# Kernel tuning notes

Measured on AMD Instinct MI355X. Metric: run time of the kernel, lower is better.

Reference implementation:

```python
import jax, jax.numpy as jnp
import numpy as np

D_MODEL = 1024
NUM_HEADS = 16
HEAD_DIM = D_MODEL // NUM_HEADS


def setup_inputs() -> dict:
    key = jax.random.key(0)
    ks = jax.random.split(key, 11)
    B, S = 4, 2048
    s = 1.0 / np.sqrt(D_MODEL)
    inp = {
        'query': jax.random.normal(ks[0], (B, S, D_MODEL), jnp.float32),
        'key': jax.random.normal(ks[1], (B, S, D_MODEL), jnp.float32),
        'value': jax.random.normal(ks[2], (B, S, D_MODEL), jnp.float32),
        'W_q': jax.random.normal(ks[3], (D_MODEL, D_MODEL), jnp.float32) * s,
        'b_q': jnp.zeros((D_MODEL,), jnp.float32),
        'W_k': jax.random.normal(ks[4], (D_MODEL, D_MODEL), jnp.float32) * s,
        'b_k': jnp.zeros((D_MODEL,), jnp.float32),
        'W_v': jax.random.normal(ks[5], (D_MODEL, D_MODEL), jnp.float32) * s,
        'b_v': jnp.zeros((D_MODEL,), jnp.float32),
        'W_o': jax.random.normal(ks[6], (D_MODEL, D_MODEL), jnp.float32) * s,
        'b_o': jnp.zeros((D_MODEL,), jnp.float32),
    }
    return inp


def reference(query, key, value, W_q, b_q, W_k, b_k, W_v, b_v, W_o, b_o):
    B, S, _ = query.shape
    # Linear projections (torch Linear: x @ W.T + b)
    Q = query @ W_q.T + b_q
    K = key @ W_k.T + b_k
    V = value @ W_v.T + b_v
    # [B, H, S, Dh]
    def split_heads(x):
        return x.reshape(B, -1, NUM_HEADS, HEAD_DIM).transpose(0, 2, 1, 3)
    Qh, Kh, Vh = split_heads(Q), split_heads(K), split_heads(V)
    scale = 1.0 / jnp.sqrt(jnp.float32(HEAD_DIM))
    scores = jnp.einsum('bhqd,bhkd->bhqk', Qh, Kh) * scale
    attn = jax.nn.softmax(scores, axis=-1)
    out = jnp.einsum('bhqk,bhkd->bhqd', attn, Vh)
    out = out.transpose(0, 2, 1, 3).reshape(B, S, D_MODEL)
    return out @ W_o.T + b_o
```

## Files before the change

### kernel.cpp

```cpp
#include <hip/hip_runtime.h>


#define BATCH 4
#define SEQ   2048
#define NH    16
#define DH    64
#define DM    1024
#define LOG2E 1.4426950408889634f
#define CSC   (0.125f * LOG2E)

typedef __attribute__((ext_vector_type(8))) short s16x8;
typedef __attribute__((ext_vector_type(4))) float f32x4;
typedef const __attribute__((address_space(1))) unsigned int* gas1;
typedef __attribute__((address_space(3))) unsigned int* las3;

__device__ __forceinline__ unsigned short f2bf(float f) {
  unsigned int u = __float_as_uint(f);
  u += 0x7FFFu + ((u >> 16) & 1u);
  return (unsigned short)(u >> 16);
}

__device__ __forceinline__ unsigned int cvt_pk_bf16(float lo, float hi) {
  unsigned int r;
  asm("v_cvt_pk_bf16_f32 %0, %1, %2" : "=v"(r) : "v"(lo), "v"(hi));
  return r;
}

__global__ __launch_bounds__(256) void cvt3_k(const float* __restrict__ s0,
                                              const float* __restrict__ s1,
                                              const float* __restrict__ s2,
                                              unsigned short* __restrict__ d0,
                                              unsigned short* __restrict__ d1,
                                              unsigned short* __restrict__ d2, int n4) {
  const float* s = blockIdx.y == 0 ? s0 : blockIdx.y == 1 ? s1 : s2;
  unsigned short* d = blockIdx.y == 0 ? d0 : blockIdx.y == 1 ? d1 : d2;
  int i = blockIdx.x * 256 + threadIdx.x;
  if (i < n4) {
    float4 v = ((const float4*)s)[i];
    ushort4 o;
    o.x = f2bf(v.x); o.y = f2bf(v.y); o.z = f2bf(v.z); o.w = f2bf(v.w);
    ((ushort4*)d)[i] = o;
  }
}

__global__ __launch_bounds__(256) void cvt4_k(const float* __restrict__ s0,
                                              const float* __restrict__ s1,
                                              const float* __restrict__ s2,
                                              const float* __restrict__ s3,
                                              unsigned short* __restrict__ d0,
                                              unsigned short* __restrict__ d1,
                                              unsigned short* __restrict__ d2,
                                              unsigned short* __restrict__ d3, int n4) {
  const float* s = blockIdx.y == 0 ? s0 : blockIdx.y == 1 ? s1 : blockIdx.y == 2 ? s2 : s3;
  unsigned short* d = blockIdx.y == 0 ? d0 : blockIdx.y == 1 ? d1 : blockIdx.y == 2 ? d2 : d3;
  int i = blockIdx.x * 256 + threadIdx.x;
  if (i < n4) {
    float4 v = ((const float4*)s)[i];
    ushort4 o;
    o.x = f2bf(v.x); o.y = f2bf(v.y); o.z = f2bf(v.z); o.w = f2bf(v.w);
    ((ushort4*)d)[i] = o;
  }
}

template<bool BIAS_ROW, bool OUT_F32>
__device__ __forceinline__ void gemm_core(const unsigned short* __restrict__ A,
                                          const unsigned short* __restrict__ Bm,
                                          const float* __restrict__ bias,
                                          void* __restrict__ Cout,
                                          int M, int N, int K, int tM, int tN,
                                          unsigned short* As, unsigned short* Bs) {
  const int tid = threadIdx.x;
  const int wave = tid >> 6, lane = tid & 63;
  const int lr = lane & 15, lh = lane >> 4;
  const int wm = (wave >> 1) * 64, wn = (wave & 1) * 64;
  f32x4 acc[4][4] = {};

  for (int k0 = 0; k0 < K; k0 += 64) {
    __syncthreads();
#pragma unroll
    for (int i = 0; i < 4; ++i) {
      const int slot = wave * 256 + i * 64 + lane;
      const int row = slot >> 3;
      const int cg = (slot & 7) ^ (row & 7);
      const unsigned short* ga = A  + (size_t)(tM * 128 + row) * K + k0 + cg * 8;
      const unsigned short* gb = Bm + (size_t)(tN * 128 + row) * K + k0 + cg * 8;
      __builtin_amdgcn_global_load_lds((gas1)ga, (las3)(As + (wave * 256 + i * 64) * 8), 16, 0, 0);
      __builtin_amdgcn_global_load_lds((gas1)gb, (las3)(Bs + (wave * 256 + i * 64) * 8), 16, 0, 0);
    }
    __syncthreads();

    s16x8 af[4][2], bfr[4][2];
#pragma unroll
    for (int mt = 0; mt < 4; ++mt) {
#pragma unroll
      for (int kt = 0; kt < 2; ++kt) {
        const int ra = wm + mt * 16 + lr;
        af[mt][kt] = *(const s16x8*)(As + ra * 64 + (((kt * 4 + lh) ^ (ra & 7)) * 8));
        const int rb = wn + mt * 16 + lr;
        bfr[mt][kt] = *(const s16x8*)(Bs + rb * 64 + (((kt * 4 + lh) ^ (rb & 7)) * 8));
      }
    }
#pragma unroll
    for (int mt = 0; mt < 4; ++mt) {
#pragma unroll
      for (int nt = 0; nt < 4; ++nt) {
        acc[mt][nt] = __builtin_amdgcn_mfma_f32_16x16x32_bf16(af[mt][0], bfr[nt][0], acc[mt][nt], 0, 0, 0);
        acc[mt][nt] = __builtin_amdgcn_mfma_f32_16x16x32_bf16(af[mt][1], bfr[nt][1], acc[mt][nt], 0, 0, 0);
      }
    }
  }

#pragma unroll
  for (int mt = 0; mt < 4; ++mt) {
#pragma unroll
    for (int nt = 0; nt < 4; ++nt) {
      const int row0 = tM * 128 + wm + mt * 16 + lh * 4;
      const int col  = tN * 128 + wn + nt * 16 + lr;
      const float bc = BIAS_ROW ? 0.f : bias[col];
#pragma unroll
      for (int r = 0; r < 4; ++r) {
        const float v = acc[mt][nt][r] + (BIAS_ROW ? bias[row0 + r] : bc);
        if (OUT_F32) ((float*)Cout)[(size_t)(row0 + r) * N + col] = v;
        else ((unsigned short*)Cout)[(size_t)(row0 + r) * N + col] = f2bf(v);
      }
    }
  }
}

template<bool BIAS_ROW, bool OUT_F32>
__global__ __launch_bounds__(256) void gemm_bt(const unsigned short* __restrict__ A,
                                               const unsigned short* __restrict__ Bm,
                                               const float* __restrict__ bias,
                                               void* __restrict__ Cout, int M, int N, int K) {
  __shared__ unsigned short As[128 * 64];
  __shared__ unsigned short Bs[128 * 64];
  gemm_core<BIAS_ROW, OUT_F32>(A, Bm, bias, Cout, M, N, K, blockIdx.y, blockIdx.x, As, Bs);
}

__global__ __launch_bounds__(256) void gemm_qk(const unsigned short* __restrict__ A0,
                                               const unsigned short* __restrict__ A1,
                                               const unsigned short* __restrict__ W0,
                                               const unsigned short* __restrict__ W1,
                                               const float* __restrict__ c0,
                                               const float* __restrict__ c1,
                                               void* __restrict__ C0, void* __restrict__ C1,
                                               int M, int N, int K) {
  __shared__ unsigned short As[128 * 64];
  __shared__ unsigned short Bs[128 * 64];
  if (blockIdx.z == 0)
    gemm_core<false, false>(A0, W0, c0, C0, M, N, K, blockIdx.y, blockIdx.x, As, Bs);
  else
    gemm_core<false, false>(A1, W1, c1, C1, M, N, K, blockIdx.y, blockIdx.x, As, Bs);
}

__global__ __launch_bounds__(256) void attn_k(const unsigned short* __restrict__ Q,
                                              const unsigned short* __restrict__ Kp,
                                              const unsigned short* __restrict__ Vt,
                                              unsigned short* __restrict__ AO) {
  __shared__ unsigned short Ks[2][64 * 64];
  __shared__ unsigned short Vs[2][64 * 64];
  __shared__ unsigned short Ps[4 * 32 * 64];
  const int tid = threadIdx.x;
  const int w = tid >> 6, lane = tid & 63;
  const int lr = lane & 15, lh = lane >> 4;
  const int sw = lr & 7;

  const int id = blockIdx.x;
  const int g  = (id & 7) * 128 + (id >> 3);
  const int qt = g & 15;
  const int hb = g >> 4;
  const int h = hb & 15, b = hb >> 4;

  s16x8 qf[2][2];
#pragma unroll
  for (int qb = 0; qb < 2; ++qb)
#pragma unroll
    for (int kt = 0; kt < 2; ++kt)
      qf[qb][kt] = *(const s16x8*)(Q + (size_t)(b * SEQ + qt * 128 + w * 32 + qb * 16 + lr) * DM
                                     + h * DH + kt * 32 + lh * 8);
  asm volatile("s_waitcnt vmcnt(0)" ::: "memory");
  __builtin_amdgcn_sched_barrier(0);

  f32x4 o[2][4] = {};
  float m_run[2] = {-1e30f, -1e30f};
  float l_run[2] = {0.f, 0.f};
  unsigned short* Pw = Ps + w * 2048;

  const unsigned short* Kbase = Kp + (size_t)b * SEQ * DM + h * DH;
  const unsigned short* Vbase = Vt + (size_t)h * DH * (BATCH * SEQ) + (size_t)b * SEQ;

  auto stage = [&](int buf, int kv0) {
#pragma unroll
    for (int i = 0; i < 2; ++i) {
      const int slot = i * 256 + w * 64 + lane;
      const int row = slot >> 3;
      const int cg = (slot & 7) ^ (row & 7);
      const unsigned short* gk = Kbase + (size_t)(kv0 + row) * DM + cg * 8;
      const unsigned short* gv = Vbase + (size_t)row * (BATCH * SEQ) + kv0 + cg * 8;
      __builtin_amdgcn_global_load_lds((gas1)gk, (las3)(&Ks[buf][(i * 256 + w * 64) * 8]), 16, 0, 0);
      __builtin_amdgcn_global_load_lds((gas1)gv, (las3)(&Vs[buf][(i * 256 + w * 64) * 8]), 16, 0, 0);
    }
  };

  stage(0, 0);
  for (int t = 0; t < 32; ++t) {
    const int cur = t & 1;
    if (t < 31) {
      stage(cur ^ 1, (t + 1) * 64);
      asm volatile("s_waitcnt vmcnt(4)" ::: "memory");
    } else {
      asm volatile("s_waitcnt vmcnt(0)" ::: "memory");
    }
    __builtin_amdgcn_s_barrier();
    __builtin_amdgcn_sched_barrier(0);
    const unsigned short* Kc = Ks[cur];
    const unsigned short* Vc = Vs[cur];

    f32x4 s[2][4] = {};
#pragma unroll
    for (int nt = 0; nt < 4; ++nt) {
#pragma unroll
      for (int kt = 0; kt < 2; ++kt) {
        const s16x8 kf = *(const s16x8*)(Kc + (nt * 16 + lr) * 64 + (((kt * 4 + lh) ^ sw) * 8));
        s[0][nt] = __builtin_amdgcn_mfma_f32_16x16x32_bf16(kf, qf[0][kt], s[0][nt], 0, 0, 0);
        s[1][nt] = __builtin_amdgcn_mfma_f32_16x16x32_bf16(kf, qf[1][kt], s[1][nt], 0, 0, 0);
      }
    }

#pragma unroll
    for (int qb = 0; qb < 2; ++qb) {
      float mx = fmaxf(fmaxf(s[qb][0][0], s[qb][0][1]), fmaxf(s[qb][0][2], s[qb][0][3]));
#pragma unroll
      for (int nt = 1; nt < 4; ++nt)
        mx = fmaxf(mx, fmaxf(fmaxf(s[qb][nt][0], s[qb][nt][1]),
                             fmaxf(s[qb][nt][2], s[qb][nt][3])));
      mx = fmaxf(mx, __shfl_xor(mx, 16));
      mx = fmaxf(mx, __shfl_xor(mx, 32));
      if (!__all(mx - m_run[qb] <= 64.0f)) {
        const float al = __builtin_amdgcn_exp2f((m_run[qb] - mx) * CSC);
        m_run[qb] = mx;
        l_run[qb] *= al;
#pragma unroll
        for (int dt = 0; dt < 4; ++dt) o[qb][dt] *= al;
      }
      const float base = m_run[qb] * CSC;
      float p[4][4];
      float rs = 0.f;
#pragma unroll
      for (int nt = 0; nt < 4; ++nt)
#pragma unroll
        for (int r = 0; r < 4; ++r) {
          p[nt][r] = __builtin_amdgcn_exp2f(s[qb][nt][r] * CSC - base);
          rs += p[nt][r];
        }
      rs += __shfl_xor(rs, 16);
      rs += __shfl_xor(rs, 32);
      l_run[qb] += rs;

      const int qrow = qb * 16 + lr;
#pragma unroll
      for (int nt = 0; nt < 4; ++nt) {
        uint2 wd;
        wd.x = cvt_pk_bf16(p[nt][0], p[nt][1]);
        wd.y = cvt_pk_bf16(p[nt][2], p[nt][3]);
        const int c8 = nt * 2 + (lh >> 1);
        *(uint2*)(Pw + qrow * 64 + (((c8 ^ sw) << 3) | ((lh & 1) << 2))) = wd;
      }
    }

#pragma unroll
    for (int nb = 0; nb < 2; ++nb) {
      const s16x8 pf0 = *(const s16x8*)(Pw + lr * 64        + (((nb * 4 + lh) ^ sw) * 8));
      const s16x8 pf1 = *(const s16x8*)(Pw + (16 + lr) * 64 + (((nb * 4 + lh) ^ sw) * 8));
#pragma unroll
      for (int dt = 0; dt < 4; ++dt) {
        const s16x8 vf = *(const s16x8*)(Vc + (dt * 16 + lr) * 64 + (((nb * 4 + lh) ^ sw) * 8));
        o[0][dt] = __builtin_amdgcn_mfma_f32_16x16x32_bf16(vf, pf0, o[0][dt], 0, 0, 0);
        o[1][dt] = __builtin_amdgcn_mfma_f32_16x16x32_bf16(vf, pf1, o[1][dt], 0, 0, 0);
      }
    }
    __builtin_amdgcn_sched_barrier(0);
    __builtin_amdgcn_s_barrier();
  }

#pragma unroll
  for (int qb = 0; qb < 2; ++qb) {
    const float rl = __builtin_amdgcn_rcpf(l_run[qb]);
    unsigned short* orow = AO + (size_t)(b * SEQ + qt * 128 + w * 32 + qb * 16 + lr) * DM + h * DH;
#pragma unroll
    for (int dt = 0; dt < 4; ++dt) {
      *(unsigned int*)(orow + dt * 16 + lh * 4)     = cvt_pk_bf16(o[qb][dt][0] * rl, o[qb][dt][1] * rl);
      *(unsigned int*)(orow + dt * 16 + lh * 4 + 2) = cvt_pk_bf16(o[qb][dt][2] * rl, o[qb][dt][3] * rl);
    }
  }
}

extern "C" void kernel_launch(void* const* d_in, const int* in_sizes, int n_in,
                              void* d_out, int out_size, void* d_ws, size_t ws_size,
                              hipStream_t stream) {
  const float* q   = (const float*)d_in[0];
  const float* k   = (const float*)d_in[1];
  const float* v   = (const float*)d_in[2];
  const float* W_q = (const float*)d_in[3];
  const float* b_q = (const float*)d_in[4];
  const float* W_k = (const float*)d_in[5];
  const float* b_k = (const float*)d_in[6];
  const float* W_v = (const float*)d_in[7];
  const float* b_v = (const float*)d_in[8];
  const float* W_o = (const float*)d_in[9];
  const float* b_o = (const float*)d_in[10];

  const size_t SD  = (size_t)BATCH * SEQ * DM;
  const size_t SDB = SD * 2;
  const size_t D2  = (size_t)DM * DM;
  if (ws_size < 5 * SDB + D2 * 2) return;

  char* base = (char*)d_ws;
  unsigned short* B0 = (unsigned short*)(base);
  unsigned short* B1 = (unsigned short*)(base + 1 * SDB);
  unsigned short* B2 = (unsigned short*)(base + 2 * SDB);
  unsigned short* B3 = (unsigned short*)(base + 3 * SDB);
  unsigned short* B4 = (unsigned short*)(base + 4 * SDB);
  unsigned short* Wb = (unsigned short*)(base + 5 * SDB);

  unsigned short* dW0 = (unsigned short*)d_out;
  unsigned short* dW1 = dW0 + D2;
  unsigned short* dW2 = dW0 + 2 * D2;

  const int nSD4 = (int)(SD / 4), nD24 = (int)(D2 / 4);
  const dim3 blk(256);

  cvt3_k<<<dim3(nSD4 / 256, 3), blk, 0, stream>>>(q, k, v, B0, B1, B2, nSD4);
  cvt4_k<<<dim3(nD24 / 256, 4), blk, 0, stream>>>(W_q, W_k, W_v, W_o, dW0, dW1, dW2, Wb, nD24);
  gemm_qk<<<dim3(DM / 128, (BATCH * SEQ) / 128, 2), blk, 0, stream>>>(
      B0, B1, dW0, dW1, b_q, b_k, B3, B4, BATCH * SEQ, DM, DM);
  gemm_bt<true, false><<<dim3((BATCH * SEQ) / 128, DM / 128), blk, 0, stream>>>(
      dW2, B2, b_v, B1, DM, BATCH * SEQ, DM);
  attn_k<<<dim3(16 * NH * BATCH), blk, 0, stream>>>(B3, B4, B1, B0);
  gemm_bt<false, true><<<dim3(DM / 128, (BATCH * SEQ) / 128), blk, 0, stream>>>(
      B0, Wb, b_o, d_out, BATCH * SEQ, DM, DM);
}
```

Measured before the change: 244.4 us.

## Halve P scratch buffer, add occupancy hint, setprio around MFMAs, precompute staging pointers

The attention kernel gets a launch-bounds hint of 4 blocks per CU and halves the per-wave P buffer in LDS by writing and consuming P in two 32-column halves with a new swizzle. It wraps the MFMA sections in s_setprio, precomputes global load pointers for K/V staging, and vectorizes the max and sum reductions. The aim is more resident blocks through lower LDS and register use, plus better overlap of MFMA with exp work. The tighter register budget may cause spills, and the split P write/read adds extra LDS round trips.

```diff
diff --git a/kernel.cpp b/kernel.cpp
--- a/kernel.cpp
+++ b/kernel.cpp
@@ -23,6 +23,13 @@
 __device__ __forceinline__ unsigned int cvt_pk_bf16(float lo, float hi) {
   unsigned int r;
   asm("v_cvt_pk_bf16_f32 %0, %1, %2" : "=v"(r) : "v"(lo), "v"(hi));
+  return r;
+}
+
+__device__ __forceinline__ f32x4 vmax4(f32x4 a, f32x4 b) {
+  f32x4 r;
+  r[0] = fmaxf(a[0], b[0]); r[1] = fmaxf(a[1], b[1]);
+  r[2] = fmaxf(a[2], b[2]); r[3] = fmaxf(a[3], b[3]);
   return r;
 }
 
@@ -153,17 +160,18 @@
     gemm_core<false, false>(A1, W1, c1, C1, M, N, K, blockIdx.y, blockIdx.x, As, Bs);
 }
 
-__global__ __launch_bounds__(256) void attn_k(const unsigned short* __restrict__ Q,
-                                              const unsigned short* __restrict__ Kp,
-                                              const unsigned short* __restrict__ Vt,
-                                              unsigned short* __restrict__ AO) {
+__global__ __launch_bounds__(256, 4) void attn_k(const unsigned short* __restrict__ Q,
+                                                 const unsigned short* __restrict__ Kp,
+                                                 const unsigned short* __restrict__ Vt,
+                                                 unsigned short* __restrict__ AO) {
   __shared__ unsigned short Ks[2][64 * 64];
   __shared__ unsigned short Vs[2][64 * 64];
-  __shared__ unsigned short Ps[4 * 32 * 64];
+  __shared__ unsigned short Ps[4 * 32 * 32];
   const int tid = threadIdx.x;
   const int w = tid >> 6, lane = tid & 63;
   const int lr = lane & 15, lh = lane >> 4;
   const int sw = lr & 7;
+  const int sp = lr & 3;
 
   const int id = blockIdx.x;
   const int g  = (id & 7) * 128 + (id >> 3);
@@ -184,29 +192,33 @@
   f32x4 o[2][4] = {};
   float m_run[2] = {-1e30f, -1e30f};
   float l_run[2] = {0.f, 0.f};
-  unsigned short* Pw = Ps + w * 2048;
+  unsigned short* Pw = Ps + w * 1024;
 
   const unsigned short* Kbase = Kp + (size_t)b * SEQ * DM + h * DH;
   const unsigned short* Vbase = Vt + (size_t)h * DH * (BATCH * SEQ) + (size_t)b * SEQ;
 
-  auto stage = [&](int buf, int kv0) {
-#pragma unroll
-    for (int i = 0; i < 2; ++i) {
-      const int slot = i * 256 + w * 64 + lane;
-      const int row = slot >> 3;
-      const int cg = (slot & 7) ^ (row & 7);
-      const unsigned short* gk = Kbase + (size_t)(kv0 + row) * DM + cg * 8;
-      const unsigned short* gv = Vbase + (size_t)row * (BATCH * SEQ) + kv0 + cg * 8;
-      __builtin_amdgcn_global_load_lds((gas1)gk, (las3)(&Ks[buf][(i * 256 + w * 64) * 8]), 16, 0, 0);
-      __builtin_amdgcn_global_load_lds((gas1)gv, (las3)(&Vs[buf][(i * 256 + w * 64) * 8]), 16, 0, 0);
-    }
+  const int slot0 = w * 64 + lane, slot1 = 256 + w * 64 + lane;
+  const int r0 = slot0 >> 3, c0 = (slot0 & 7) ^ (r0 & 7);
+  const int r1 = slot1 >> 3, c1 = (slot1 & 7) ^ (r1 & 7);
+  const unsigned short* gk0 = Kbase + (size_t)r0 * DM + c0 * 8;
+  const unsigned short* gk1 = Kbase + (size_t)r1 * DM + c1 * 8;
+  const unsigned short* gv0 = Vbase + (size_t)r0 * (BATCH * SEQ) + c0 * 8;
+  const unsigned short* gv1 = Vbase + (size_t)r1 * (BATCH * SEQ) + c1 * 8;
+  const int dst0 = (w * 64) * 8, dst1 = (256 + w * 64) * 8;
+
+  auto stage = [&](int buf) {
+    __builtin_amdgcn_global_load_lds((gas1)gk0, (las3)(&Ks[buf][dst0]), 16, 0, 0);
+    __builtin_amdgcn_global_load_lds((gas1)gk1, (las3)(&Ks[buf][dst1]), 16, 0, 0);
+    __builtin_amdgcn_global_load_lds((gas1)gv0, (las3)(&Vs[buf][dst0]), 16, 0, 0);
+    __builtin_amdgcn_global_load_lds((gas1)gv1, (las3)(&Vs[buf][dst1]), 16, 0, 0);
+    gk0 += 64 * DM; gk1 += 64 * DM; gv0 += 64; gv1 += 64;
   };
 
-  stage(0, 0);
+  stage(0);
   for (int t = 0; t < 32; ++t) {
     const int cur = t & 1;
     if (t < 31) {
-      stage(cur ^ 1, (t + 1) * 64);
+      stage(cur ^ 1);
       asm volatile("s_waitcnt vmcnt(4)" ::: "memory");
     } else {
       asm volatile("s_waitcnt vmcnt(0)" ::: "memory");
@@ -217,6 +229,7 @@
     const unsigned short* Vc = Vs[cur];
 
     f32x4 s[2][4] = {};
+    __builtin_amdgcn_s_setprio(1);
 #pragma unroll
     for (int nt = 0; nt < 4; ++nt) {
 #pragma unroll
@@ -226,14 +239,13 @@
         s[1][nt] = __builtin_amdgcn_mfma_f32_16x16x32_bf16(kf, qf[1][kt], s[1][nt], 0, 0, 0);
       }
     }
-
+    __builtin_amdgcn_s_setprio(0);
+
+    f32x4 p[2][4];
 #pragma unroll
     for (int qb = 0; qb < 2; ++qb) {
-      float mx = fmaxf(fmaxf(s[qb][0][0], s[qb][0][1]), fmaxf(s[qb][0][2], s[qb][0][3]));
-#pragma unroll
-      for (int nt = 1; nt < 4; ++nt)
-        mx = fmaxf(mx, fmaxf(fmaxf(s[qb][nt][0], s[qb][nt][1]),
-                             fmaxf(s[qb][nt][2], s[qb][nt][3])));
+      const f32x4 m03 = vmax4(vmax4(s[qb][0], s[qb][1]), vmax4(s[qb][2], s[qb][3]));
+      float mx = fmaxf(fmaxf(m03[0], m03[1]), fmaxf(m03[2], m03[3]));
       mx = fmaxf(mx, __shfl_xor(mx, 16));
       mx = fmaxf(mx, __shfl_xor(mx, 32));
       if (!__all(mx - m_run[qb] <= 64.0f)) {
@@ -244,40 +256,43 @@
         for (int dt = 0; dt < 4; ++dt) o[qb][dt] *= al;
       }
       const float base = m_run[qb] * CSC;
-      float p[4][4];
-      float rs = 0.f;
 #pragma unroll
       for (int nt = 0; nt < 4; ++nt)
 #pragma unroll
-        for (int r = 0; r < 4; ++r) {
-          p[nt][r] = __builtin_amdgcn_exp2f(s[qb][nt][r] * CSC - base);
-          rs += p[nt][r];
-        }
+        for (int r = 0; r < 4; ++r)
+          p[qb][nt][r] = __builtin_amdgcn_exp2f(s[qb][nt][r] * CSC - base);
+      const f32x4 st = (p[qb][0] + p[qb][1]) + (p[qb][2] + p[qb][3]);
+      float rs = (st[0] + st[1]) + (st[2] + st[3]);
       rs += __shfl_xor(rs, 16);
       rs += __shfl_xor(rs, 32);
       l_run[qb] += rs;
-
-      const int qrow = qb * 16 + lr;
-#pragma unroll
-      for (int nt = 0; nt < 4; ++nt) {
-        uint2 wd;
-        wd.x = cvt_pk_bf16(p[nt][0], p[nt][1]);
-        wd.y = cvt_pk_bf16(p[nt][2], p[nt][3]);
-        const int c8 = nt * 2 + (lh >> 1);
-        *(uint2*)(Pw + qrow * 64 + (((c8 ^ sw) << 3) | ((lh & 1) << 2))) = wd;
-      }
-    }
-
-#pragma unroll
-    for (int nb = 0; nb < 2; ++nb) {
-      const s16x8 pf0 = *(const s16x8*)(Pw + lr * 64        + (((nb * 4 + lh) ^ sw) * 8));
-      const s16x8 pf1 = *(const s16x8*)(Pw + (16 + lr) * 64 + (((nb * 4 + lh) ^ sw) * 8));
+    }
+
+#pragma unroll
+    for (int hf = 0; hf < 2; ++hf) {
+#pragma unroll
+      for (int qb = 0; qb < 2; ++qb) {
+        const int row = qb * 16 + lr;
+#pragma unroll
+        for (int ntl = 0; ntl < 2; ++ntl) {
+          const int nt = hf * 2 + ntl;
+          uint2 wd;
+          wd.x = cvt_pk_bf16(p[qb][nt][0], p[qb][nt][1]);
+          wd.y = cvt_pk_bf16(p[qb][nt][2], p[qb][nt][3]);
+          const int cc = (ntl * 4 + lh) ^ (sp << 1);
+          *(uint2*)(Pw + row * 32 + cc * 4) = wd;
+        }
+      }
+      __builtin_amdgcn_s_setprio(1);
+      const s16x8 pf0 = *(const s16x8*)(Pw + lr * 32        + ((lh ^ sp) * 8));
+      const s16x8 pf1 = *(const s16x8*)(Pw + (16 + lr) * 32 + ((lh ^ sp) * 8));
 #pragma unroll
       for (int dt = 0; dt < 4; ++dt) {
-        const s16x8 vf = *(const s16x8*)(Vc + (dt * 16 + lr) * 64 + (((nb * 4 + lh) ^ sw) * 8));
+        const s16x8 vf = *(const s16x8*)(Vc + (dt * 16 + lr) * 64 + (((hf * 4 + lh) ^ sw) * 8));
         o[0][dt] = __builtin_amdgcn_mfma_f32_16x16x32_bf16(vf, pf0, o[0][dt], 0, 0, 0);
         o[1][dt] = __builtin_amdgcn_mfma_f32_16x16x32_bf16(vf, pf1, o[1][dt], 0, 0, 0);
       }
+      __builtin_amdgcn_s_setprio(0);
     }
     __builtin_amdgcn_sched_barrier(0);
     __builtin_amdgcn_s_barrier();
```

New measurement: 235.8 us. 3.5% less time.
